# Optimization experiments

Hardware: AMD Instinct MI355X
Metric: run time of the kernel (lower is better)

The kernel has to match this reference:

```python
import jax, jax.numpy as jnp
import numpy as np

ANGSTROM_TO_BOHR = 1.8897261258369282
CUTOFF = 5.2  # angstrom
N_SPECIES = 4  # H, C, N, O

# GFN1-xTB-style per-element constants for (H, C, N, O)
_ALPHA = np.array([2.209700, 1.247655, 1.524329, 1.845886], dtype=np.float32)
_Y_EFF = np.array([1.116244, 4.428763, 5.498808, 5.171786], dtype=np.float32)


def _smooth_cutoff(d, rc, eps=1e-10):
    # torchani 'smooth' cutoff: exp(1 - 1/(1 - (d/rc)^2)) for d < rc, else 0
    x2 = (d / rc) ** 2
    e = 1.0 - 1.0 / jnp.maximum(1.0 - x2, eps)
    return jnp.where(d < rc, jnp.exp(e), jnp.zeros_like(d))


def setup_inputs() -> dict:
    key = jax.random.key(0)
    k1, k2, k3 = jax.random.split(key, 3)
    M, A, P = 2048, 64, 8388608
    element_idxs = jax.random.randint(k1, (M, A), 0, N_SPECIES, dtype=jnp.int64)
    neighbor_idxs = jax.random.randint(k2, (2, P), 0, M * A, dtype=jnp.int64)
    distances = jax.random.uniform(k3, (P,), dtype=jnp.float32, minval=0.5, maxval=6.0)
    # precomputed pairwise parameter tables (buffers in the torch module)
    y_ab = jnp.asarray(np.outer(_Y_EFF, _Y_EFF))                 # [4,4]
    sqrt_alpha_ab = jnp.asarray(np.sqrt(np.outer(_ALPHA, _ALPHA)))  # [4,4]
    k_rep = np.full((N_SPECIES, N_SPECIES), 1.5, dtype=np.float32)
    k_rep[0, 0] = 1.0  # H-H
    k_rep_ab = jnp.asarray(k_rep)
    return {
        "element_idxs": element_idxs,
        "neighbor_idxs": neighbor_idxs,
        "distances": distances,
        "y_ab": y_ab,
        "sqrt_alpha_ab": sqrt_alpha_ab,
        "k_rep_ab": k_rep_ab,
    }


def reference(element_idxs, neighbor_idxs, distances, y_ab, sqrt_alpha_ab, k_rep_ab):
    M, A = element_idxs.shape
    d = jnp.clip(distances, 1e-7) * ANGSTROM_TO_BOHR  # [P] bohr
    species12 = element_idxs.reshape(-1)[neighbor_idxs]  # [2, P]
    s0, s1 = species12[0], species12[1]
    y = y_ab[s0, s1]                    # [P] gather
    sa = sqrt_alpha_ab[s0, s1]          # [P]
    kr = k_rep_ab[s0, s1]               # [P]
    rep = (y / d) * jnp.exp(-sa * d ** kr)
    rep = rep * _smooth_cutoff(d, CUTOFF * ANGSTROM_TO_BOHR)
    mol_idx = neighbor_idxs[0] // A     # [P]
    energies = jax.ops.segment_sum(rep, mol_idx, num_segments=M)  # [M]
    return energies
```

## Files before the change

kernel.cpp:

```cpp
#include <hip/hip_runtime.h>


#define AB_D 1.8897261258369282

__global__ __launch_bounds__(256) void pack_zero_kernel(
    const int* __restrict__ elem, int natoms, int nwords,
    unsigned* __restrict__ packed, float* __restrict__ out, int M)
{
    int g = blockIdx.x * blockDim.x + threadIdx.x;
    if (g < M) out[g] = 0.0f;
    if (packed != nullptr && g < nwords) {
        int base = g * 16;
        unsigned w = 0u;
        if (base + 16 <= natoms) {
            const int4* p = (const int4*)(elem + base);
            #pragma unroll
            for (int q = 0; q < 4; ++q) {
                int4 v = p[q];
                w |= ((unsigned)v.x & 3u) << (2 * (4 * q + 0));
                w |= ((unsigned)v.y & 3u) << (2 * (4 * q + 1));
                w |= ((unsigned)v.z & 3u) << (2 * (4 * q + 2));
                w |= ((unsigned)v.w & 3u) << (2 * (4 * q + 3));
            }
        } else {
            for (int j = 0; j < 16; ++j) {
                int a = base + j;
                unsigned s = (a < natoms) ? ((unsigned)elem[a] & 3u) : 0u;
                w |= s << (2 * j);
            }
        }
        packed[g] = w;
    }
}

__device__ __forceinline__ float sel4(unsigned s, float a, float b, float c, float d)
{
    float lo = (s & 1u) ? b : a;
    float hi = (s & 1u) ? d : c;
    return (s & 2u) ? hi : lo;
}

__global__ __launch_bounds__(512, 6) void rep_main_kernel(
    const int* __restrict__ nbr, const float* __restrict__ dist,
    const unsigned* __restrict__ packed_g,
    const float* __restrict__ y_ab, const float* __restrict__ sa_ab,
    const float* __restrict__ kr_ab,
    long long P, int M, int nwords, int ashift, int A,
    float* __restrict__ partials, float* __restrict__ out,
    int mode )
{
    extern __shared__ char smem[];
    float* acc = (float*)smem;
    size_t acc_bytes = ((size_t)M * 4 + 255) & ~(size_t)255;
    unsigned* pk = (unsigned*)(smem + acc_bytes);

    const int tid = threadIdx.x;
    const int nthr = blockDim.x;

    for (int m = tid; m < M; m += nthr) acc[m] = 0.0f;
    for (int w = tid; w < nwords; w += nthr) pk[w] = packed_g[w];

    const float yv0 = sqrtf(y_ab[0]),  yv1 = sqrtf(y_ab[5]);
    const float yv2 = sqrtf(y_ab[10]), yv3 = sqrtf(y_ab[15]);
    const float av0 = sqrtf(sa_ab[0]),  av1 = sqrtf(sa_ab[5]);
    const float av2 = sqrtf(sa_ab[10]), av3 = sqrtf(sa_ab[15]);
    const float krHH = kr_ab[0];
    const float krXX = kr_ab[5];
    __syncthreads();

    const float ABf   = (float)AB_D;
    const float RC    = (float)(5.2 * AB_D);
    const float RCINV = (float)(1.0 / (5.2 * AB_D));
    const int* nb0 = nbr;
    const int* nb1 = nbr + P;

    auto process = [&](int a0, int a1, float draw) {
        float d = fmaxf(draw, 1e-7f) * ABf;
        if (d < RC) {
            unsigned ua0 = (unsigned)a0, ua1 = (unsigned)a1;
            unsigned w0 = pk[ua0 >> 4];
            unsigned w1 = pk[ua1 >> 4];
            unsigned s0 = (w0 >> ((ua0 & 15u) * 2u)) & 3u;
            unsigned s1 = (w1 >> ((ua1 & 15u) * 2u)) & 3u;

            float y  = sel4(s0, yv0, yv1, yv2, yv3) * sel4(s1, yv0, yv1, yv2, yv3);
            float sa = sel4(s0, av0, av1, av2, av3) * sel4(s1, av0, av1, av2, av3);
            float kr = ((s0 | s1) == 0u) ? krHH : krXX;

            float drep = __powf(d, kr);
            float x    = d * RCINV;
            float om   = fmaf(-x, x, 1.0f);
            float e    = 1.0f - __builtin_amdgcn_rcpf(fmaxf(om, 1e-10f));
            float rep  = y * __builtin_amdgcn_rcpf(d) * __expf(fmaf(-sa, drep, e));

            unsigned mol = (ashift >= 0) ? (ua0 >> ashift) : (ua0 / (unsigned)A);
            atomicAdd(&acc[mol], rep);
        }
    };

    long long P4 = P >> 2;
    long long gstride = (long long)gridDim.x * nthr;
    for (long long q = (long long)blockIdx.x * nthr + tid; q < P4; q += gstride) {
        int4   i0 = ((const int4*)nb0)[q];
        int4   i1 = ((const int4*)nb1)[q];
        float4 dv = ((const float4*)dist)[q];
        process(i0.x, i1.x, dv.x);
        process(i0.y, i1.y, dv.y);
        process(i0.z, i1.z, dv.z);
        process(i0.w, i1.w, dv.w);
    }
    long long tail0 = P4 << 2;
    if (blockIdx.x == 0) {
        for (long long p = tail0 + tid; p < P; p += nthr)
            process(nb0[p], nb1[p], dist[p]);
    }
    __syncthreads();

    if (mode == 0) {
        float* row = partials + (size_t)blockIdx.x * (size_t)M;
        for (int m = tid; m < M; m += nthr) row[m] = acc[m];
    } else {
        for (int m = tid; m < M; m += nthr) {
            float v = acc[m];
            if (v != 0.0f) atomicAdd(&out[m], v);
        }
    }
}

__global__ __launch_bounds__(256) void reduce_kernel(
    const float* __restrict__ partials, float* __restrict__ out,
    int M, int nblk, int rows_per)
{
    int m = blockIdx.x * blockDim.x + threadIdx.x;
    if (m >= M) return;
    int r0 = blockIdx.y * rows_per;
    int r1 = r0 + rows_per;
    if (r1 > nblk) r1 = nblk;
    if (r0 >= r1) return;
    float s0 = 0.f, s1 = 0.f, s2 = 0.f, s3 = 0.f;
    int r = r0;
    for (; r + 3 < r1; r += 4) {
        s0 += partials[(size_t)(r + 0) * M + m];
        s1 += partials[(size_t)(r + 1) * M + m];
        s2 += partials[(size_t)(r + 2) * M + m];
        s3 += partials[(size_t)(r + 3) * M + m];
    }
    for (; r < r1; ++r) s0 += partials[(size_t)r * M + m];
    atomicAdd(&out[m], (s0 + s1) + (s2 + s3));
}

extern "C" void kernel_launch(void* const* d_in, const int* in_sizes, int n_in,
                              void* d_out, int out_size, void* d_ws, size_t ws_size,
                              hipStream_t stream)
{
    const int*   elem  = (const int*)d_in[0];
    const int*   nbr   = (const int*)d_in[1];
    const float* dist  = (const float*)d_in[2];
    const float* y_ab  = (const float*)d_in[3];
    const float* sa_ab = (const float*)d_in[4];
    const float* kr_ab = (const float*)d_in[5];
    float* out = (float*)d_out;

    const int natoms = in_sizes[0];
    const long long P = (long long)in_sizes[2];
    const int M = out_size;
    const int A = natoms / M;
    int ashift = -1;
    if (A > 0 && (A & (A - 1)) == 0) {
        int s = 0;
        while ((1 << s) < A) ++s;
        ashift = s;
    }
    const int nwords = (natoms + 15) / 16;

    size_t packed_bytes = ((size_t)nwords * 4 + 255) & ~(size_t)255;
    bool have_packed = (ws_size >= packed_bytes);
    unsigned* packed = have_packed ? (unsigned*)d_ws : nullptr;
    if (!have_packed) return;

    const int BLOCK = 512;
    int nblk = 768;
    float* partials = nullptr;
    int mode = 1;
    {
        size_t avail = ws_size - packed_bytes;
        size_t rowb = (size_t)M * 4;
        long long maxrows = (long long)(avail / rowb);
        if (maxrows >= 64) {
            nblk = (int)(maxrows < 768 ? maxrows : 768);
            partials = (float*)((char*)d_ws + packed_bytes);
            mode = 0;
        }
    }

    {
        int total = (nwords > M) ? nwords : M;
        int g = (total + 255) / 256;
        hipLaunchKernelGGL(pack_zero_kernel, dim3(g), dim3(256), 0, stream,
                           elem, natoms, nwords, packed, out, M);
    }

    {
        size_t acc_bytes = ((size_t)M * 4 + 255) & ~(size_t)255;
        size_t smem = acc_bytes + (size_t)nwords * 4;
        hipLaunchKernelGGL(rep_main_kernel, dim3(nblk), dim3(BLOCK), smem, stream,
                           nbr, dist, packed, y_ab, sa_ab, kr_ab,
                           P, M, nwords, ashift, A, partials, out, mode);
    }

    if (mode == 0) {
        const int SPLIT = 32;
        int rows_per = (nblk + SPLIT - 1) / SPLIT;
        dim3 grid((M + 255) / 256, SPLIT);
        hipLaunchKernelGGL(reduce_kernel, grid, dim3(256), 0, stream,
                           partials, out, M, nblk, rows_per);
    }
}
```

Baseline: 163.6 us.

## Replace powf with sqrt-based exponent and LDS pair table, enlarge blocks

Swaps the general pow(d, kr) for a sqrt multiply, which is only valid because kr is 1.0 or 1.5; the kr==1 case is encoded as the sign of a prescaled sqrt_alpha entry. The select chains are replaced by a 16-entry LDS table of (y, sa*log2e), and exp2 is used directly with log2e folded into the constants. The eps clamp on the cutoff denominator is dropped, and blocks change from 512 to 1024 threads with 512 blocks. The aim is to cut transcendental and ALU work per pair, at the cost of assuming kr is only 1 or 1.5 and adding an extra LDS load per pair.

Result: faster. 154.0 us (-5.9%).

```diff
diff --git a/kernel.cpp b/kernel.cpp
--- a/kernel.cpp
+++ b/kernel.cpp
@@ -2,6 +2,7 @@
 
 
 #define AB_D 1.8897261258369282
+#define L2E  1.4426950408889634f
 
 __global__ __launch_bounds__(256) void pack_zero_kernel(
     const int* __restrict__ elem, int natoms, int nwords,
@@ -33,14 +34,7 @@
     }
 }
 
-__device__ __forceinline__ float sel4(unsigned s, float a, float b, float c, float d)
-{
-    float lo = (s & 1u) ? b : a;
-    float hi = (s & 1u) ? d : c;
-    return (s & 2u) ? hi : lo;
-}
-
-__global__ __launch_bounds__(512, 6) void rep_main_kernel(
+__global__ __launch_bounds__(1024, 8) void rep_main_kernel(
     const int* __restrict__ nbr, const float* __restrict__ dist,
     const unsigned* __restrict__ packed_g,
     const float* __restrict__ y_ab, const float* __restrict__ sa_ab,
@@ -50,48 +44,49 @@
     int mode )
 {
     extern __shared__ char smem[];
-    float* acc = (float*)smem;
-    size_t acc_bytes = ((size_t)M * 4 + 255) & ~(size_t)255;
-    unsigned* pk = (unsigned*)(smem + acc_bytes);
+    float*  acc = (float*)smem;
+    float2* tbl = (float2*)(smem + (size_t)M * 4);
+    unsigned* pk = (unsigned*)(smem + (size_t)M * 4 + 16 * sizeof(float2));
 
     const int tid = threadIdx.x;
     const int nthr = blockDim.x;
 
     for (int m = tid; m < M; m += nthr) acc[m] = 0.0f;
     for (int w = tid; w < nwords; w += nthr) pk[w] = packed_g[w];
-
-    const float yv0 = sqrtf(y_ab[0]),  yv1 = sqrtf(y_ab[5]);
-    const float yv2 = sqrtf(y_ab[10]), yv3 = sqrtf(y_ab[15]);
-    const float av0 = sqrtf(sa_ab[0]),  av1 = sqrtf(sa_ab[5]);
-    const float av2 = sqrtf(sa_ab[10]), av3 = sqrtf(sa_ab[15]);
-    const float krHH = kr_ab[0];
-    const float krXX = kr_ab[5];
+    if (tid < 16) {
+        float sa = sa_ab[tid] * L2E;
+        if (kr_ab[tid] == 1.0f) sa = -sa;
+        tbl[tid] = make_float2(y_ab[tid], sa);
+    }
     __syncthreads();
 
-    const float ABf   = (float)AB_D;
-    const float RC    = (float)(5.2 * AB_D);
-    const float RCINV = (float)(1.0 / (5.2 * AB_D));
+    const float ABf    = (float)AB_D;
+    const float DMIN   = (float)(1e-7 * AB_D);
+    const float RC     = (float)(5.2 * AB_D);
+    const float RCINV  = (float)(1.0 / (5.2 * AB_D));
     const int* nb0 = nbr;
     const int* nb1 = nbr + P;
 
     auto process = [&](int a0, int a1, float draw) {
-        float d = fmaxf(draw, 1e-7f) * ABf;
+        float d = fmaxf(draw * ABf, DMIN);
         if (d < RC) {
             unsigned ua0 = (unsigned)a0, ua1 = (unsigned)a1;
             unsigned w0 = pk[ua0 >> 4];
             unsigned w1 = pk[ua1 >> 4];
             unsigned s0 = (w0 >> ((ua0 & 15u) * 2u)) & 3u;
             unsigned s1 = (w1 >> ((ua1 & 15u) * 2u)) & 3u;
-
-            float y  = sel4(s0, yv0, yv1, yv2, yv3) * sel4(s1, yv0, yv1, yv2, yv3);
-            float sa = sel4(s0, av0, av1, av2, av3) * sel4(s1, av0, av1, av2, av3);
-            float kr = ((s0 | s1) == 0u) ? krHH : krXX;
-
-            float drep = __powf(d, kr);
+            float2 t = tbl[s0 * 4u + s1];
+
+            float sq   = __builtin_amdgcn_sqrtf(d);
+            float fac  = (t.y < 0.0f) ? 1.0f : sq;
+            float drep = d * fac;
             float x    = d * RCINV;
             float om   = fmaf(-x, x, 1.0f);
-            float e    = 1.0f - __builtin_amdgcn_rcpf(fmaxf(om, 1e-10f));
-            float rep  = y * __builtin_amdgcn_rcpf(d) * __expf(fmaf(-sa, drep, e));
+            float r    = __builtin_amdgcn_rcpf(om);
+            float e    = fmaf(-L2E, r, L2E);
+            float arg  = fmaf(-fabsf(t.y), drep, e);
+            float ex   = __builtin_amdgcn_exp2f(arg);
+            float rep  = t.x * __builtin_amdgcn_rcpf(d) * ex;
 
             unsigned mol = (ashift >= 0) ? (ua0 >> ashift) : (ua0 / (unsigned)A);
             atomicAdd(&acc[mol], rep);
@@ -178,8 +173,8 @@
     unsigned* packed = have_packed ? (unsigned*)d_ws : nullptr;
     if (!have_packed) return;
 
-    const int BLOCK = 512;
-    int nblk = 768;
+    const int BLOCK = 1024;
+    int nblk = 512;
     float* partials = nullptr;
     int mode = 1;
     {
@@ -187,7 +182,7 @@
         size_t rowb = (size_t)M * 4;
         long long maxrows = (long long)(avail / rowb);
         if (maxrows >= 64) {
-            nblk = (int)(maxrows < 768 ? maxrows : 768);
+            nblk = (int)(maxrows < 512 ? maxrows : 512);
             partials = (float*)((char*)d_ws + packed_bytes);
             mode = 0;
         }
@@ -201,8 +196,7 @@
     }
 
     {
-        size_t acc_bytes = ((size_t)M * 4 + 255) & ~(size_t)255;
-        size_t smem = acc_bytes + (size_t)nwords * 4;
+        size_t smem = (size_t)M * 4 + 16 * sizeof(float2) + (size_t)nwords * 4;
         hipLaunchKernelGGL(rep_main_kernel, dim3(nblk), dim3(BLOCK), smem, stream,
                            nbr, dist, packed, y_ab, sa_ab, kr_ab,
                            P, M, nwords, ashift, A, partials, out, mode);
```
